# Kernel tuning notes

Measured on AMD Instinct MI355X. Metric: run time of the kernel, lower is better.

Reference implementation:

```python
import jax, jax.numpy as jnp
import numpy as np

N = 100000      # nodes
E = 1600000     # edges (avg degree 16)
IN = 128
H = 128
OUT = 64
L = 4


def setup_inputs() -> dict:
    key = jax.random.key(0)
    ks = jax.random.split(key, 12)
    x = jax.random.normal(ks[0], (N, IN), dtype=jnp.float32)
    edge_index = jax.random.randint(ks[1], (2, E), 0, N, dtype=jnp.int64)
    def glorot(k, shp):
        return jax.random.normal(k, shp, dtype=jnp.float32) * (1.0 / np.sqrt(shp[0]))
    inp = {"x": x, "edge_index": edge_index}
    dims = [(IN, H), (H, H), (H, H), (H, H)]
    for i, (fi, fo) in enumerate(dims):
        inp[f"W{i}"] = glorot(ks[2 + i], (fi, fo))
        inp[f"b{i}"] = jnp.zeros((fo,), dtype=jnp.float32)
    inp["lin_W"] = glorot(ks[10], (L * H, OUT))
    inp["lin_b"] = jnp.zeros((OUT,), dtype=jnp.float32)
    return inp


def reference(x, W0, b0, W1, b1, W2, b2, W3, b3, lin_W, lin_b, edge_index):
    # GCN with self-loops and symmetric normalization D^-1/2 (A+I) D^-1/2
    loop = jnp.arange(N, dtype=edge_index.dtype)
    src = jnp.concatenate([edge_index[0], loop])  # [E+N]
    dst = jnp.concatenate([edge_index[1], loop])  # [E+N]
    deg = jax.ops.segment_sum(jnp.ones_like(dst, dtype=x.dtype), dst, N)  # [N]
    dinv = jnp.where(deg > 0, jax.lax.rsqrt(deg), 0.0)
    ew = dinv[src] * dinv[dst]  # per-edge norm [E+N]

    params = [(W0, b0), (W1, b1), (W2, b2), (W3, b3)]
    xs = []
    h = x
    for W, b in params:
        h = h @ W                                            # [N, H]
        msg = h[src] * ew[:, None]                           # gather [E+N, H]
        h = jax.ops.segment_sum(msg, dst, N) + b             # scatter-add [N, H]
        h = jax.nn.relu(h)                                   # dropout p=0 -> identity
        xs.append(h)
    jk = jnp.concatenate(xs, axis=-1)                        # [N, L*H]
    logits = jk @ lin_W + lin_b                              # [N, OUT]
    return jax.nn.log_softmax(logits, axis=-1)
```

## Files before the change

kernel.cpp:

```cpp
#include <hip/hip_runtime.h>
#include <cstdint>
#include <cstddef>

#define NN 100000
#define NE 1600000
#define NTOT (NE + NN)
#define HF 128
#define OF 64
#define SHARD 12500
#define BCHUNK 2048
#define BCAP 210000
#define KB 32


typedef short bfrag_t __attribute__((ext_vector_type(8)));
typedef float f4v     __attribute__((ext_vector_type(4)));


__device__ __forceinline__ unsigned int f2bf_rne(float f) {
    unsigned int u = __float_as_uint(f);
    return (u + 0x7fffu + ((u >> 16) & 1u)) >> 16;
}
__device__ __forceinline__ unsigned int pack_bf2(float lo, float hi) {
    return f2bf_rne(lo) | (f2bf_rne(hi) << 16);
}


__global__ __launch_bounds__(64) void k_init(int* gcnt) {
    if (threadIdx.x < 8) gcnt[threadIdx.x] = 0;
}

__device__ __forceinline__ int nt_load(const int* p) {
    return __builtin_nontemporal_load(p);
}

__global__ __launch_bounds__(256) void k_bin(const int* __restrict__ ei,
                                             int* __restrict__ gcnt,
                                             uint2* __restrict__ binbuf) {
    __shared__ uint2 bins[8][640];
    __shared__ int cnt[8], base[8], anynz;
    int tid = threadIdx.x;
    if (tid < 8) cnt[tid] = 0;
    if (tid == 0) anynz = 0;
    __syncthreads();
    int ebeg = blockIdx.x * BCHUNK;
    int eend = min(NE, ebeg + BCHUNK);
    int v = 0;
    for (int e = ebeg + tid; e < eend; e += 256) v |= nt_load(&ei[2 * e + 1]);
    if (v) anynz = 1;
    __syncthreads();
    bool is64 = (anynz == 0);
    for (int e = ebeg + tid; e < eend; e += 256) {
        int d = is64 ? nt_load(&ei[2 * (NE + e)]) : nt_load(&ei[NE + e]);
        int s = is64 ? nt_load(&ei[2 * e])        : nt_load(&ei[e]);
        int x = (unsigned)d / SHARD;
        int p = atomicAdd(&cnt[x], 1);
        if (p < 640) bins[x][p] = make_uint2((unsigned)d, (unsigned)s);
    }
    __syncthreads();
    if (tid < 8) {
        int c = min(cnt[tid], 640);
        cnt[tid] = c;
        base[tid] = atomicAdd(&gcnt[tid], c);
    }
    __syncthreads();
    for (int x = 0; x < 8; ++x) {
        int c = cnt[x], b0 = base[x];
        for (int i = tid; i < c; i += 256)
            if (b0 + i < BCAP) binbuf[(size_t)x * BCAP + b0 + i] = bins[x][i];
    }
}

__global__ __launch_bounds__(256) void k_cnt(const int* __restrict__ gcnt,
                                             const uint2* __restrict__ binbuf,
                                             int* __restrict__ blockhist) {
    __shared__ int hist[SHARD];
    int tid = threadIdx.x;
    int x = blockIdx.x & 7, kb = blockIdx.x >> 3;
    int n = min(gcnt[x], BCAP);
    int chunk = (n + KB - 1) / KB;
    int beg = kb * chunk, end = min(n, beg + chunk);
    for (int i = tid; i < SHARD; i += 256) hist[i] = 0;
    __syncthreads();
    for (int i = beg + tid; i < end; i += 256) {
        uint2 r = binbuf[(size_t)x * BCAP + i];
        atomicAdd(&hist[r.x - (unsigned)x * SHARD], 1);
    }
    __syncthreads();
    int* bh = blockhist + ((size_t)x * KB + kb) * SHARD;
    for (int i = tid; i < SHARD; i += 256) bh[i] = hist[i];
}

__global__ __launch_bounds__(256) void k_colscan(int* __restrict__ blockhist,
                                                 int* __restrict__ deg) {
    int i = blockIdx.x * 256 + threadIdx.x;
    if (i >= NN) return;
    int x = i / SHARD, ln = i % SHARD;
    int* col = blockhist + (size_t)x * KB * SHARD + ln;
    int s = 0;
#pragma unroll
    for (int kb = 0; kb < KB; ++kb) {
        int c = col[(size_t)kb * SHARD];
        col[(size_t)kb * SHARD] = s;
        s += c;
    }
    deg[i] = 1 + s;
}

__global__ __launch_bounds__(256) void k_scanA(const int* deg, int* rowptr, int* bsum,
                                               float* dinv) {
    __shared__ int sh[256];
    int tid = threadIdx.x;
    int base = blockIdx.x * 1024 + tid * 4;
    int v0 = 0, v1 = 0, v2 = 0, v3 = 0;
    if (base + 0 < NN) v0 = deg[base + 0];
    if (base + 1 < NN) v1 = deg[base + 1];
    if (base + 2 < NN) v2 = deg[base + 2];
    if (base + 3 < NN) v3 = deg[base + 3];
    if (base + 0 < NN) dinv[base + 0] = rsqrtf((float)v0);
    if (base + 1 < NN) dinv[base + 1] = rsqrtf((float)v1);
    if (base + 2 < NN) dinv[base + 2] = rsqrtf((float)v2);
    if (base + 3 < NN) dinv[base + 3] = rsqrtf((float)v3);
    int s = v0 + v1 + v2 + v3;
    sh[tid] = s;
    __syncthreads();
    for (int off = 1; off < 256; off <<= 1) {
        int t = (tid >= off) ? sh[tid - off] : 0;
        __syncthreads();
        sh[tid] += t;
        __syncthreads();
    }
    int run = sh[tid] - s;
    if (base + 0 < NN) rowptr[base + 0] = run; run += v0;
    if (base + 1 < NN) rowptr[base + 1] = run; run += v1;
    if (base + 2 < NN) rowptr[base + 2] = run; run += v2;
    if (base + 3 < NN) rowptr[base + 3] = run;
    if (tid == 255) bsum[blockIdx.x] = sh[255];
}

__global__ __launch_bounds__(128) void k_scanB(const int* bsum, int* boff, int* rowptr) {
    __shared__ int sh[128];
    int tid = threadIdx.x;
    int v = (tid < 98) ? bsum[tid] : 0;
    sh[tid] = v;
    __syncthreads();
    for (int off = 1; off < 128; off <<= 1) {
        int t = (tid >= off) ? sh[tid - off] : 0;
        __syncthreads();
        sh[tid] += t;
        __syncthreads();
    }
    if (tid < 98) boff[tid] = sh[tid] - v;
    if (tid == 0) rowptr[NN] = NTOT;
}

__global__ __launch_bounds__(256) void k_scanC(int* rowptr, const int* boff, int* csr) {
    int i = blockIdx.x * 256 + threadIdx.x;
    if (i < NN) {
        int r = rowptr[i] + boff[i >> 10];
        rowptr[i] = r;
        csr[r] = i;
    }
}

__global__ __launch_bounds__(256) void k_fill(const int* __restrict__ gcnt,
                                              const uint2* __restrict__ binbuf,
                                              const int* __restrict__ blockhist,
                                              const int* __restrict__ rowptr,
                                              int* __restrict__ csr) {
    __shared__ int lrank[SHARD];
    int tid = threadIdx.x;
    int x = blockIdx.x & 7, kb = blockIdx.x >> 3;
    int n = min(gcnt[x], BCAP);
    int chunk = (n + KB - 1) / KB;
    int beg = kb * chunk, end = min(n, beg + chunk);
    for (int i = tid; i < SHARD; i += 256) lrank[i] = 0;
    __syncthreads();
    const int* bh = blockhist + ((size_t)x * KB + kb) * SHARD;
    for (int i = beg + tid; i < end; i += 256) {
        uint2 r = binbuf[(size_t)x * BCAP + i];
        int ln = r.x - (unsigned)x * SHARD;
        int lr = atomicAdd(&lrank[ln], 1);
        csr[rowptr[r.x] + 1 + bh[ln] + lr] = (int)r.y;
    }
}

__global__ __launch_bounds__(256) void k_xcvt(const float* __restrict__ x,
                                              uint4* __restrict__ xb4) {
    int t = blockIdx.x * 256 + threadIdx.x;
    if (t >= NN * 16) return;
    int row = t >> 4, lj = t & 15;
    const float* xr = x + (size_t)row * 128 + lj;
    uint4 o;
    o.x = pack_bf2(xr[0],  xr[16]);
    o.y = pack_bf2(xr[32], xr[48]);
    o.z = pack_bf2(xr[64], xr[80]);
    o.w = pack_bf2(xr[96], xr[112]);
    xb4[(size_t)row * 16 + lj] = o;
}

__global__ __launch_bounds__(256) void k_prep(const float* __restrict__ W0,
                                              const float* __restrict__ W1,
                                              const float* __restrict__ W2,
                                              const float* __restrict__ W3,
                                              const float* __restrict__ linW,
                                              unsigned short* __restrict__ WT,
                                              unsigned short* __restrict__ WjT) {
    int idx = blockIdx.x * 256 + threadIdx.x;
    if (idx < 4 * 128 * 128) {
        int l = idx >> 14, r = idx & 16383, n = r >> 7, p = r & 127;
        int c = (p & 7) * 16 + (p >> 3);
        const float* Wl = (l == 0) ? W0 : (l == 1) ? W1 : (l == 2) ? W2 : W3;
        WT[idx] = (unsigned short)f2bf_rne(Wl[c * 128 + n]);
    } else if (idx < 4 * 128 * 128 + 4 * 64 * 128) {
        int i2 = idx - 65536;
        int l = i2 >> 13, r = i2 & 8191, n = r >> 7, p = r & 127;
        int c = (p & 7) * 16 + (p >> 3);
        WjT[i2] = (unsigned short)f2bf_rne(linW[(size_t)(l * 128 + c) * 64 + n]);
    }
}

__global__ __launch_bounds__(256) void k_mmf(const unsigned short* __restrict__ A,
                                             const unsigned short* __restrict__ WT,
                                             const float* __restrict__ dinv,
                                             uint4* __restrict__ m4o) {
    __shared__ unsigned short Wlds[128 * 128];
    int tid = threadIdx.x;
    int row0 = blockIdx.x * 64;

    for (int c = tid; c < 2048; c += 256) {
        int row = c >> 4, c16 = c & 15;
        uint4 v = *(const uint4*)&WT[row * 128 + c16 * 8];
        *(uint4*)((char*)Wlds + row * 256 + ((c16 * 16) ^ ((row & 7) << 4))) = v;
    }

    int lane = tid & 63, w = tid >> 6;
    int r15 = lane & 15, q = lane >> 4;
    int xo = (r15 & 7) << 4;

    int arow = row0 + 16 * w + r15;
    bool av = arow < NN;
    bfrag_t afr[4];
#pragma unroll
    for (int ks = 0; ks < 4; ++ks) {
        bfrag_t z = {0, 0, 0, 0, 0, 0, 0, 0};
        afr[ks] = av ? *(const bfrag_t*)&A[(size_t)arow * 128 + ks * 32 + q * 8] : z;
    }
    __syncthreads();

    f4v acc[8];
#pragma unroll
    for (int i = 0; i < 8; ++i) acc[i] = (f4v){0.f, 0.f, 0.f, 0.f};

#pragma unroll
    for (int ks = 0; ks < 4; ++ks) {
        int ko = ks * 64 + q * 16;
#pragma unroll
        for (int nb = 0; nb < 8; ++nb) {
            bfrag_t b = *(const bfrag_t*)((const char*)Wlds + (nb * 16 + r15) * 256 + (ko ^ xo));
            acc[nb] = __builtin_amdgcn_mfma_f32_16x16x32_bf16(afr[ks], b, acc[nb], 0, 0, 0);
        }
    }

#pragma unroll
    for (int reg = 0; reg < 4; ++reg) {
        int gr = row0 + 16 * w + q * 4 + reg;
        if (gr < NN) {
            float sc = dinv[gr];
            uint4 o;
            o.x = pack_bf2(acc[0][reg] * sc, acc[1][reg] * sc);
            o.y = pack_bf2(acc[2][reg] * sc, acc[3][reg] * sc);
            o.z = pack_bf2(acc[4][reg] * sc, acc[5][reg] * sc);
            o.w = pack_bf2(acc[6][reg] * sc, acc[7][reg] * sc);
            m4o[(size_t)gr * 16 + r15] = o;
        }
    }
}

__global__ __launch_bounds__(256) void k_agg(const int* __restrict__ rowptr,
                                             const int* __restrict__ csr,
                                             const uint4* __restrict__ m4,
                                             const float* __restrict__ dinv,
                                             const float* __restrict__ bias,
                                             uint4* __restrict__ outb) {
    int w = threadIdx.x >> 6, lane = threadIdx.x & 63;
    int grp = lane >> 4, lj = lane & 15;
    int node = blockIdx.x * 4 + w;
    if (node >= NN) return;
    int beg = rowptr[node], end = rowptr[node + 1];

    float a[8];
#pragma unroll
    for (int q = 0; q < 8; ++q) a[q] = 0.f;

    auto acc8 = [&](uint4 v) {
        a[0] += __uint_as_float(v.x << 16);
        a[1] += __uint_as_float(v.x & 0xffff0000u);
        a[2] += __uint_as_float(v.y << 16);
        a[3] += __uint_as_float(v.y & 0xffff0000u);
        a[4] += __uint_as_float(v.z << 16);
        a[5] += __uint_as_float(v.z & 0xffff0000u);
        a[6] += __uint_as_float(v.w << 16);
        a[7] += __uint_as_float(v.w & 0xffff0000u);
    };

    for (int base = beg; base < end; base += 64) {
        int cnt = min(64, end - base);
        int sv = (lane < cnt) ? csr[base + lane] : 0;
        int k = 0;
        for (; k + 16 <= cnt; k += 16) {
            int s0 = __shfl(sv, k + grp);
            int s1 = __shfl(sv, k + 4 + grp);
            int s2 = __shfl(sv, k + 8 + grp);
            int s3 = __shfl(sv, k + 12 + grp);
            uint4 v0 = m4[(size_t)s0 * 16 + lj];
            uint4 v1 = m4[(size_t)s1 * 16 + lj];
            uint4 v2 = m4[(size_t)s2 * 16 + lj];
            uint4 v3 = m4[(size_t)s3 * 16 + lj];
            acc8(v0); acc8(v1); acc8(v2); acc8(v3);
        }
        for (; k + 4 <= cnt; k += 4) {
            int s = __shfl(sv, k + grp);
            uint4 v = m4[(size_t)s * 16 + lj];
            acc8(v);
        }
        int rem = cnt - k;
        if (rem) {
            int idx = k + grp;
            if (idx >= cnt) idx = cnt - 1;
            int s = __shfl(sv, idx);
            if (grp < rem) {
                uint4 v = m4[(size_t)s * 16 + lj];
                acc8(v);
            }
        }
    }
#pragma unroll
    for (int q = 0; q < 8; ++q) a[q] += __shfl_xor(a[q], 16);
#pragma unroll
    for (int q = 0; q < 8; ++q) a[q] += __shfl_xor(a[q], 32);

    if (grp == 0) {
        float sc = dinv[node];
        float r[8];
#pragma unroll
        for (int q = 0; q < 8; ++q)
            r[q] = fmaxf(a[q] * sc + bias[q * 16 + lj], 0.f);
        uint4 o;
        o.x = pack_bf2(r[0], r[1]);
        o.y = pack_bf2(r[2], r[3]);
        o.z = pack_bf2(r[4], r[5]);
        o.w = pack_bf2(r[6], r[7]);
        outb[(size_t)node * 16 + lj] = o;
    }
}

__global__ __launch_bounds__(256) void k_jk4(const unsigned short* __restrict__ h0,
                                             const unsigned short* __restrict__ h1,
                                             const unsigned short* __restrict__ h2,
                                             const unsigned short* __restrict__ h3,
                                             const unsigned short* __restrict__ WjT,
                                             const float* __restrict__ linb,
                                             float* __restrict__ out) {
    __shared__ unsigned short Wjlds[4 * 64 * 128];
    int tid = threadIdx.x;
    int row0 = blockIdx.x * 64;

    for (int c = tid; c < 4096; c += 256) {
        int row = c >> 4, c16 = c & 15;
        uint4 v = *(const uint4*)&WjT[row * 128 + c16 * 8];
        *(uint4*)((char*)Wjlds + row * 256 + ((c16 * 16) ^ ((row & 7) << 4))) = v;
    }

    int lane = tid & 63, w = tid >> 6;
    int r15 = lane & 15, q = lane >> 4;
    int xo = (r15 & 7) << 4;
    int arow = row0 + 16 * w + r15;
    bool av = arow < NN;
    const unsigned short* hs[4] = {h0, h1, h2, h3};

    __syncthreads();

    f4v accj[4];
#pragma unroll
    for (int i = 0; i < 4; ++i) accj[i] = (f4v){0.f, 0.f, 0.f, 0.f};

#pragma unroll
    for (int l = 0; l < 4; ++l) {
        bfrag_t afr[4];
#pragma unroll
        for (int ks = 0; ks < 4; ++ks) {
            bfrag_t z = {0, 0, 0, 0, 0, 0, 0, 0};
            afr[ks] = av ? *(const bfrag_t*)&hs[l][(size_t)arow * 128 + ks * 32 + q * 8] : z;
        }
#pragma unroll
        for (int ks = 0; ks < 4; ++ks) {
            int ko = ks * 64 + q * 16;
#pragma unroll
            for (int jb = 0; jb < 4; ++jb) {
                bfrag_t b = *(const bfrag_t*)((const char*)Wjlds
                            + (l * 64 + jb * 16 + r15) * 256 + (ko ^ xo));
                accj[jb] = __builtin_amdgcn_mfma_f32_16x16x32_bf16(afr[ks], b, accj[jb], 0, 0, 0);
            }
        }
    }

#pragma unroll
    for (int reg = 0; reg < 4; ++reg) {
        int gr = row0 + 16 * w + q * 4 + reg;
        float v0 = accj[0][reg] + linb[r15];
        float v1 = accj[1][reg] + linb[16 + r15];
        float v2 = accj[2][reg] + linb[32 + r15];
        float v3 = accj[3][reg] + linb[48 + r15];
        float mx = fmaxf(fmaxf(v0, v1), fmaxf(v2, v3));
#pragma unroll
        for (int s = 1; s < 16; s <<= 1) mx = fmaxf(mx, __shfl_xor(mx, s, 16));
        float sum = expf(v0 - mx) + expf(v1 - mx) + expf(v2 - mx) + expf(v3 - mx);
#pragma unroll
        for (int s = 1; s < 16; s <<= 1) sum += __shfl_xor(sum, s, 16);
        float ls = logf(sum) + mx;
        if (gr < NN) {
            out[(size_t)gr * 64 + r15]      = v0 - ls;
            out[(size_t)gr * 64 + 16 + r15] = v1 - ls;
            out[(size_t)gr * 64 + 32 + r15] = v2 - ls;
            out[(size_t)gr * 64 + 48 + r15] = v3 - ls;
        }
    }
}


extern "C" void kernel_launch(void* const* d_in, const int* in_sizes, int n_in,
                              void* d_out, int out_size, void* d_ws, size_t ws_size,
                              hipStream_t stream) {
    const float* x    = (const float*)d_in[0];
    const int*   ei   = (const int*)d_in[1];
    const float* W[4] = {(const float*)d_in[2], (const float*)d_in[4],
                         (const float*)d_in[6], (const float*)d_in[8]};
    const float* b[4] = {(const float*)d_in[3], (const float*)d_in[5],
                         (const float*)d_in[7], (const float*)d_in[9]};
    const float* linW = (const float*)d_in[10];
    const float* linb = (const float*)d_in[11];
    float* out = (float*)d_out;

    char* wp = (char*)d_ws;
    auto alloc = [&](size_t bytes) {
        void* p = (void*)wp;
        wp += (bytes + 255) & ~(size_t)255;
        return p;
    };
    int*   gcnt    = (int*)  alloc(32);
    int*   deg     = (int*)  alloc((size_t)NN * 4);
    float* dinv    = (float*)alloc((size_t)NN * 4);
    int*   rowptr  = (int*)  alloc((size_t)(NN + 1) * 4);
    int*   bsum    = (int*)  alloc(512);
    int*   boff    = (int*)  alloc(512);
    int*   csr     = (int*)  alloc((size_t)NTOT * 4);
    uint2* binbuf  = (uint2*)alloc((size_t)8 * BCAP * 8);
    int*   blockhist = (int*)alloc((size_t)8 * KB * SHARD * 4);
    unsigned short* WT  = (unsigned short*)alloc((size_t)4 * 128 * 128 * 2);
    unsigned short* WjT = (unsigned short*)alloc((size_t)4 * 64 * 128 * 2);
    unsigned short* xb   = (unsigned short*)alloc((size_t)NN * 128 * 2);
    unsigned short* bufM = (unsigned short*)alloc((size_t)NN * 128 * 2);
    unsigned short* h[4];
    for (int l = 0; l < 4; ++l)
        h[l] = (unsigned short*)alloc((size_t)NN * 128 * 2);

    dim3 blk(256);
    k_init   <<<1, dim3(64), 0, stream>>>(gcnt);
    k_prep   <<<384, blk, 0, stream>>>(W[0], W[1], W[2], W[3], linW, WT, WjT);
    k_xcvt   <<<6250, blk, 0, stream>>>(x, (uint4*)xb);
    k_bin    <<<(NE + BCHUNK - 1) / BCHUNK, blk, 0, stream>>>(ei, gcnt, binbuf);
    k_cnt    <<<8 * KB, blk, 0, stream>>>(gcnt, binbuf, blockhist);
    k_colscan<<<391, blk, 0, stream>>>(blockhist, deg);
    k_scanA  <<<98, blk, 0, stream>>>(deg, rowptr, bsum, dinv);
    k_scanB  <<<1, dim3(128), 0, stream>>>(bsum, boff, rowptr);
    k_scanC  <<<391, blk, 0, stream>>>(rowptr, boff, csr);
    k_fill   <<<8 * KB, blk, 0, stream>>>(gcnt, binbuf, blockhist, rowptr, csr);

    const unsigned short* lin[4] = {xb, h[0], h[1], h[2]};
    for (int l = 0; l < 4; ++l) {
        k_mmf<<<1563, blk, 0, stream>>>(lin[l], WT + (size_t)l * 128 * 128, dinv,
                                        (uint4*)bufM);
        k_agg<<<25000, blk, 0, stream>>>(rowptr, csr, (const uint4*)bufM, dinv,
                                         b[l], (uint4*)h[l]);
    }
    k_jk4<<<1563, blk, 0, stream>>>(h[0], h[1], h[2], h[3], WjT, linb, out);
}
```

Before: 451.7 us.

## Chunk feature layout by 16 columns and pin each aggregation chunk to one XCD

Activations move from row-major [N,128] bf16 to 8 column chunks of 16 features, each stored as a contiguous [N,16] slab. The matmul, input-conversion and JK kernels read and write this layout. The aggregation kernel now assigns chunk index blockIdx&7 to each block, so with round-robin block dispatch each XCD gathers only from one slab of about 3.2 MB, which should fit in its L2. The trade-off is narrower 8-byte gathers per lane, each block looping over 8 nodes per wave, and repeated reads of rowptr and csr once per chunk.

```diff
diff --git a/kernel.cpp b/kernel.cpp
--- a/kernel.cpp
+++ b/kernel.cpp
@@ -196,7 +196,7 @@
     o.y = pack_bf2(xr[32], xr[48]);
     o.z = pack_bf2(xr[64], xr[80]);
     o.w = pack_bf2(xr[96], xr[112]);
-    xb4[(size_t)row * 16 + lj] = o;
+    xb4[((size_t)(lj >> 1) * NN + row) * 2 + (lj & 1)] = o;
 }
 
 __global__ __launch_bounds__(256) void k_prep(const float* __restrict__ W0,
@@ -220,6 +220,12 @@
     }
 }
 
+__device__ __forceinline__ const bfrag_t* frag_addr(const unsigned short* A,
+                                                    int arow, int ks, int q) {
+    return (const bfrag_t*)&A[((size_t)(2 * ks + (q >> 1)) * NN + arow) * 16
+                              + (q & 1) * 8];
+}
+
 __global__ __launch_bounds__(256) void k_mmf(const unsigned short* __restrict__ A,
                                              const unsigned short* __restrict__ WT,
                                              const float* __restrict__ dinv,
@@ -244,7 +250,7 @@
 #pragma unroll
     for (int ks = 0; ks < 4; ++ks) {
         bfrag_t z = {0, 0, 0, 0, 0, 0, 0, 0};
-        afr[ks] = av ? *(const bfrag_t*)&A[(size_t)arow * 128 + ks * 32 + q * 8] : z;
+        afr[ks] = av ? *frag_addr(A, arow, ks, q) : z;
     }
     __syncthreads();
 
@@ -272,86 +278,80 @@
             o.y = pack_bf2(acc[2][reg] * sc, acc[3][reg] * sc);
             o.z = pack_bf2(acc[4][reg] * sc, acc[5][reg] * sc);
             o.w = pack_bf2(acc[6][reg] * sc, acc[7][reg] * sc);
-            m4o[(size_t)gr * 16 + r15] = o;
+            m4o[((size_t)(r15 >> 1) * NN + gr) * 2 + (r15 & 1)] = o;
         }
     }
 }
 
 __global__ __launch_bounds__(256) void k_agg(const int* __restrict__ rowptr,
                                              const int* __restrict__ csr,
-                                             const uint4* __restrict__ m4,
+                                             const uint2* __restrict__ m2,
                                              const float* __restrict__ dinv,
                                              const float* __restrict__ bias,
-                                             uint4* __restrict__ outb) {
-    int w = threadIdx.x >> 6, lane = threadIdx.x & 63;
-    int grp = lane >> 4, lj = lane & 15;
-    int node = blockIdx.x * 4 + w;
-    if (node >= NN) return;
-    int beg = rowptr[node], end = rowptr[node + 1];
-
-    float a[8];
-#pragma unroll
-    for (int q = 0; q < 8; ++q) a[q] = 0.f;
-
-    auto acc8 = [&](uint4 v) {
-        a[0] += __uint_as_float(v.x << 16);
-        a[1] += __uint_as_float(v.x & 0xffff0000u);
-        a[2] += __uint_as_float(v.y << 16);
-        a[3] += __uint_as_float(v.y & 0xffff0000u);
-        a[4] += __uint_as_float(v.z << 16);
-        a[5] += __uint_as_float(v.z & 0xffff0000u);
-        a[6] += __uint_as_float(v.w << 16);
-        a[7] += __uint_as_float(v.w & 0xffff0000u);
-    };
-
-    for (int base = beg; base < end; base += 64) {
-        int cnt = min(64, end - base);
-        int sv = (lane < cnt) ? csr[base + lane] : 0;
-        int k = 0;
-        for (; k + 16 <= cnt; k += 16) {
-            int s0 = __shfl(sv, k + grp);
-            int s1 = __shfl(sv, k + 4 + grp);
-            int s2 = __shfl(sv, k + 8 + grp);
-            int s3 = __shfl(sv, k + 12 + grp);
-            uint4 v0 = m4[(size_t)s0 * 16 + lj];
-            uint4 v1 = m4[(size_t)s1 * 16 + lj];
-            uint4 v2 = m4[(size_t)s2 * 16 + lj];
-            uint4 v3 = m4[(size_t)s3 * 16 + lj];
-            acc8(v0); acc8(v1); acc8(v2); acc8(v3);
-        }
-        for (; k + 4 <= cnt; k += 4) {
-            int s = __shfl(sv, k + grp);
-            uint4 v = m4[(size_t)s * 16 + lj];
-            acc8(v);
-        }
-        int rem = cnt - k;
-        if (rem) {
-            int idx = k + grp;
-            if (idx >= cnt) idx = cnt - 1;
-            int s = __shfl(sv, idx);
-            if (grp < rem) {
-                uint4 v = m4[(size_t)s * 16 + lj];
-                acc8(v);
+                                             uint2* __restrict__ outb) {
+    int tid = threadIdx.x;
+    int wv = tid >> 6, lane = tid & 63;
+    int g4 = lane >> 2, l4 = lane & 3;
+    int c = blockIdx.x & 7;
+    int ng = blockIdx.x >> 3;
+    const uint2* __restrict__ mc = m2 + (size_t)c * NN * 4;
+
+    float bb[4];
+#pragma unroll
+    for (int j = 0; j < 4; ++j) {
+        int p = c * 16 + l4 * 4 + j;
+        bb[j] = bias[(p & 7) * 16 + (p >> 3)];
+    }
+
+    for (int i = 0; i < 8; ++i) {
+        int node = (ng * 4 + wv) * 8 + i;
+        int beg = nt_load(&rowptr[node]);
+        int end = nt_load(&rowptr[node + 1]);
+        float a0 = 0.f, a1 = 0.f, a2 = 0.f, a3 = 0.f;
+        for (int base = beg; base < end; base += 64) {
+            int cnt = min(64, end - base);
+            int sv = (lane < cnt) ? nt_load(&csr[base + lane]) : 0;
+            int k = 0;
+            for (; k + 16 <= cnt; k += 16) {
+                int s = __shfl(sv, k + g4);
+                uint2 v = mc[(size_t)s * 4 + l4];
+                a0 += __uint_as_float(v.x << 16);
+                a1 += __uint_as_float(v.x & 0xffff0000u);
+                a2 += __uint_as_float(v.y << 16);
+                a3 += __uint_as_float(v.y & 0xffff0000u);
             }
-        }
-    }
-#pragma unroll
-    for (int q = 0; q < 8; ++q) a[q] += __shfl_xor(a[q], 16);
-#pragma unroll
-    for (int q = 0; q < 8; ++q) a[q] += __shfl_xor(a[q], 32);
-
-    if (grp == 0) {
-        float sc = dinv[node];
-        float r[8];
-#pragma unroll
-        for (int q = 0; q < 8; ++q)
-            r[q] = fmaxf(a[q] * sc + bias[q * 16 + lj], 0.f);
-        uint4 o;
-        o.x = pack_bf2(r[0], r[1]);
-        o.y = pack_bf2(r[2], r[3]);
-        o.z = pack_bf2(r[4], r[5]);
-        o.w = pack_bf2(r[6], r[7]);
-        outb[(size_t)node * 16 + lj] = o;
+            int rem = cnt - k;
+            if (rem) {
+                int idx = k + g4;
+                if (idx >= cnt) idx = cnt - 1;
+                int s = __shfl(sv, idx);
+                if (g4 < rem) {
+                    uint2 v = mc[(size_t)s * 4 + l4];
+                    a0 += __uint_as_float(v.x << 16);
+                    a1 += __uint_as_float(v.x & 0xffff0000u);
+                    a2 += __uint_as_float(v.y << 16);
+                    a3 += __uint_as_float(v.y & 0xffff0000u);
+                }
+            }
+        }
+#pragma unroll
+        for (int off = 4; off <= 32; off <<= 1) {
+            a0 += __shfl_xor(a0, off);
+            a1 += __shfl_xor(a1, off);
+            a2 += __shfl_xor(a2, off);
+            a3 += __shfl_xor(a3, off);
+        }
+        if (g4 == 0) {
+            float sc = dinv[node];
+            float r0 = fmaxf(a0 * sc + bb[0], 0.f);
+            float r1 = fmaxf(a1 * sc + bb[1], 0.f);
+            float r2 = fmaxf(a2 * sc + bb[2], 0.f);
+            float r3 = fmaxf(a3 * sc + bb[3], 0.f);
+            uint2 o;
+            o.x = pack_bf2(r0, r1);
+            o.y = pack_bf2(r2, r3);
+            outb[((size_t)c * NN + node) * 4 + l4] = o;
+        }
     }
 }
 
@@ -391,7 +391,7 @@
 #pragma unroll
         for (int ks = 0; ks < 4; ++ks) {
             bfrag_t z = {0, 0, 0, 0, 0, 0, 0, 0};
-            afr[ks] = av ? *(const bfrag_t*)&hs[l][(size_t)arow * 128 + ks * 32 + q * 8] : z;
+            afr[ks] = av ? *frag_addr(hs[l], arow, ks, q) : z;
         }
 #pragma unroll
         for (int ks = 0; ks < 4; ++ks) {
@@ -481,8 +481,8 @@
     for (int l = 0; l < 4; ++l) {
         k_mmf<<<1563, blk, 0, stream>>>(lin[l], WT + (size_t)l * 128 * 128, dinv,
                                         (uint4*)bufM);
-        k_agg<<<25000, blk, 0, stream>>>(rowptr, csr, (const uint4*)bufM, dinv,
-                                         b[l], (uint4*)h[l]);
+        k_agg<<<25000, blk, 0, stream>>>(rowptr, csr, (const uint2*)bufM, dinv,
+                                         b[l], (uint2*)h[l]);
     }
     k_jk4<<<1563, blk, 0, stream>>>(h[0], h[1], h[2], h[3], WjT, linb, out);
 }
```

New measurement: 1.225 ms. 2.71x slower.
